# Performance work log

Measured on AMD Instinct MI355X. Metric: run time of the kernel, lower is better.

The kernel has to match this reference:

```python
import jax, jax.numpy as jnp
import numpy as np

N, HID, H, D = 2048, 1024, 16, 64


def setup_inputs() -> dict:
    key = jax.random.key(0)
    ks = jax.random.split(key, 10)
    s_in = 1.0 / np.sqrt(HID)      # Linear(hidden -> H*D) init scale
    s_o = 1.0 / np.sqrt(H * D)     # Linear(H*D -> D) init scale
    return {
        "x": jax.random.normal(ks[0], (N, HID), jnp.float32),
        "history": jnp.zeros((H, N, N), jnp.float32),
        "Wq_w": jax.random.uniform(ks[1], (H * D, HID), jnp.float32, -s_in, s_in),
        "Wq_b": jax.random.uniform(ks[2], (H * D,), jnp.float32, -s_in, s_in),
        "Wk_w": jax.random.uniform(ks[3], (H * D, HID), jnp.float32, -s_in, s_in),
        "Wk_b": jax.random.uniform(ks[4], (H * D,), jnp.float32, -s_in, s_in),
        "Wv_w": jax.random.uniform(ks[5], (H * D, HID), jnp.float32, -s_in, s_in),
        "Wv_b": jax.random.uniform(ks[6], (H * D,), jnp.float32, -s_in, s_in),
        "Wo_w": jax.random.uniform(ks[7], (D, H * D), jnp.float32, -s_o, s_o),
        "Wo_b": jax.random.uniform(ks[8], (D,), jnp.float32, -s_o, s_o),
        "beta": jnp.float32(0.1),
    }


def reference(x, history, Wq_w, Wq_b, Wk_w, Wk_b, Wv_w, Wv_b, Wo_w, Wo_b, beta):
    n = x.shape[0]
    # QKV projections: [N, H*D] -> [H, N, D]
    q = (x @ Wq_w.T + Wq_b).reshape(n, H, D).transpose(1, 0, 2)
    k = (x @ Wk_w.T + Wk_b).reshape(n, H, D).transpose(1, 0, 2)
    v = (x @ Wv_w.T + Wv_b).reshape(n, H, D).transpose(1, 0, 2)
    scores = jnp.einsum('hnd,hmd->hnm', q, k) / np.sqrt(D).astype(np.float32)
    scores = scores + beta * history  # learned additive history bias
    attn = jax.nn.softmax(scores, axis=-1)  # [H, N, N]
    new_history = history + jax.lax.stop_gradient(attn)  # stateful accumulation (detached)
    out = jnp.einsum('hnm,hmd->hnd', attn, v)  # [H, N, D]
    out = out.transpose(1, 0, 2).reshape(n, H * D)
    out = out @ Wo_w.T + Wo_b  # [N, D]
    # dropout is identity (p=0.0 / eval)
    return (out, attn, new_history)
```

## Files before the change

### kernel.cpp

```cpp
#include <hip/hip_runtime.h>
#include <hip/hip_bf16.h>

#define N_TOK 2048
#define HIDDEN 1024
#define NHEAD 16
#define DHEAD 64

typedef __attribute__((ext_vector_type(8))) short bf16x8;
typedef __attribute__((ext_vector_type(4))) float f32x4;

__device__ inline unsigned short f2bf(float x) {
    __hip_bfloat16 h = __float2bfloat16(x);
    return *reinterpret_cast<unsigned short*>(&h);
}

__device__ inline f32x4 zero4() {
    f32x4 z;
    z[0] = 0.f; z[1] = 0.f; z[2] = 0.f; z[3] = 0.f;
    return z;
}

__global__ void cvt4_kernel(const float* __restrict__ x, const float* __restrict__ wq,
                            const float* __restrict__ wk, const float* __restrict__ wv,
                            unsigned short* __restrict__ dst) {
    int i = blockIdx.x * blockDim.x + threadIdx.x;
    const float* src;
    int off;
    if (i < 524288)       { src = x;  off = i; }
    else if (i < 786432)  { src = wq; off = i - 524288; }
    else if (i < 1048576) { src = wk; off = i - 786432; }
    else                  { src = wv; off = i - 1048576; }
    float4 v = reinterpret_cast<const float4*>(src)[off];
    ushort4 o;
    o.x = f2bf(v.x); o.y = f2bf(v.y); o.z = f2bf(v.z); o.w = f2bf(v.w);
    reinterpret_cast<ushort4*>(dst)[i] = o;
}

__launch_bounds__(256)
__global__ void gemm_qkv(const unsigned short* __restrict__ xb,
                         const unsigned short* __restrict__ wb,
                         const float* __restrict__ bq, const float* __restrict__ bk,
                         const float* __restrict__ bv,
                         unsigned short* __restrict__ qb, unsigned short* __restrict__ kb,
                         unsigned short* __restrict__ vb) {
    __shared__ unsigned short As[2][128 * 64];
    __shared__ unsigned short Bs[2][128 * 64];
    const int tid = threadIdx.x;
    const int lane = tid & 63;
    const int w = tid >> 6;
    const int wr = w >> 1, wc = w & 1;
    const int rb = blockIdx.y * 128;
    const int cb = blockIdx.x * 128;
    const int r0 = tid >> 3, c0 = tid & 7;

    f32x4 acc[4][4];
    for (int i = 0; i < 4; i++)
        for (int j = 0; j < 4; j++) acc[i][j] = zero4();

    uint4 va[4], vb4[4];
#pragma unroll
    for (int i = 0; i < 4; i++) {
        va[i]  = *reinterpret_cast<const uint4*>(xb + (size_t)(rb + r0 + 32 * i) * HIDDEN + c0 * 8);
        vb4[i] = *reinterpret_cast<const uint4*>(wb + (size_t)(cb + r0 + 32 * i) * HIDDEN + c0 * 8);
    }
#pragma unroll
    for (int i = 0; i < 4; i++) {
        int row = r0 + 32 * i;
        *reinterpret_cast<uint4*>(As[0] + row * 64 + ((c0 ^ (row & 7)) << 3)) = va[i];
        *reinterpret_cast<uint4*>(Bs[0] + row * 64 + ((c0 ^ (row & 7)) << 3)) = vb4[i];
    }
    __syncthreads();
    int cur = 0;

    for (int kt = 0; kt < 16; ++kt) {
        if (kt < 15) {
#pragma unroll
            for (int i = 0; i < 4; i++) {
                va[i]  = *reinterpret_cast<const uint4*>(xb + (size_t)(rb + r0 + 32 * i) * HIDDEN + (kt + 1) * 64 + c0 * 8);
                vb4[i] = *reinterpret_cast<const uint4*>(wb + (size_t)(cb + r0 + 32 * i) * HIDDEN + (kt + 1) * 64 + c0 * 8);
            }
        }
#pragma unroll
        for (int kk = 0; kk < 2; kk++) {
            bf16x8 a[4], b[4];
#pragma unroll
            for (int mi = 0; mi < 4; mi++) {
                int row = wr * 64 + mi * 16 + (lane & 15);
                a[mi] = *reinterpret_cast<const bf16x8*>(As[cur] + row * 64 + (((kk * 4 + (lane >> 4)) ^ (row & 7)) << 3));
            }
#pragma unroll
            for (int ni = 0; ni < 4; ni++) {
                int row = wc * 64 + ni * 16 + (lane & 15);
                b[ni] = *reinterpret_cast<const bf16x8*>(Bs[cur] + row * 64 + (((kk * 4 + (lane >> 4)) ^ (row & 7)) << 3));
            }
#pragma unroll
            for (int mi = 0; mi < 4; mi++)
#pragma unroll
                for (int ni = 0; ni < 4; ni++)
                    acc[mi][ni] = __builtin_amdgcn_mfma_f32_16x16x32_bf16(a[mi], b[ni], acc[mi][ni], 0, 0, 0);
        }
        if (kt < 15) {
#pragma unroll
            for (int i = 0; i < 4; i++) {
                int row = r0 + 32 * i;
                *reinterpret_cast<uint4*>(As[cur ^ 1] + row * 64 + ((c0 ^ (row & 7)) << 3)) = va[i];
                *reinterpret_cast<uint4*>(Bs[cur ^ 1] + row * 64 + ((c0 ^ (row & 7)) << 3)) = vb4[i];
            }
        }
        __syncthreads();
        cur ^= 1;
    }

    const int region = blockIdx.x >> 3;
    const float* bias = region == 0 ? bq : (region == 1 ? bk : bv);
    unsigned short* dst = region == 0 ? qb : (region == 1 ? kb : vb);
#pragma unroll
    for (int mi = 0; mi < 4; mi++) {
#pragma unroll
        for (int ni = 0; ni < 4; ni++) {
            int colg = cb + wc * 64 + ni * 16 + (lane & 15);
            int jj = colg & 1023;
            int hh = jj >> 6, d = jj & 63;
            float bval = bias[jj];
#pragma unroll
            for (int r = 0; r < 4; r++) {
                int n = rb + wr * 64 + mi * 16 + ((lane >> 4) << 2) + r;
                dst[((size_t)hh * N_TOK + n) * 64 + d] = f2bf(acc[mi][ni][r] + bval);
            }
        }
    }
}

__global__ void transpose_v(const unsigned short* __restrict__ vb, unsigned short* __restrict__ vt) {
    int t = blockIdx.x * blockDim.x + threadIdx.x;
    int nc = t & 255, d = (t >> 8) & 63, h = t >> 14;
    int n0 = nc * 8;
    unsigned short tmp[8];
#pragma unroll
    for (int j = 0; j < 8; j++)
        tmp[j] = vb[((size_t)h * N_TOK + n0 + j) * 64 + d];
    size_t dsti = (((size_t)(h * 32 + (nc >> 3)) * 64 + d) * 64) + (nc & 7) * 8;
    *reinterpret_cast<uint4*>(vt + dsti) = *reinterpret_cast<uint4*>(tmp);
}

__launch_bounds__(64, 2)
__global__ void attn_fused(const unsigned short* __restrict__ qb,
                           const unsigned short* __restrict__ kb,
                           const unsigned short* __restrict__ vt,
                           const float* __restrict__ hist,
                           const float* __restrict__ beta_p,
                           float* __restrict__ attn_out,
                           float* __restrict__ nh_out,
                           float* __restrict__ hv) {
    __shared__ unsigned short Ks[64 * 64];
    __shared__ unsigned short Vs[64 * 64];
    __shared__ unsigned short Ps[16 * 64];
    const int lane = threadIdx.x;
    const int g = lane >> 4, q15 = lane & 15;
    const int jr8 = lane >> 3, jc = lane & 7;
    const int rb = blockIdx.x, h = blockIdx.y;
    const float beta = beta_p[0];
    const float scale = 0.125f;

    const unsigned short* qsrc = qb + ((size_t)h * N_TOK + rb * 16 + q15) * 64;
    bf16x8 aq0 = *reinterpret_cast<const bf16x8*>(qsrc + 8 * g);
    bf16x8 aq1 = *reinterpret_cast<const bf16x8*>(qsrc + 8 * g + 32);

    const unsigned short* kt0 = kb + (size_t)h * N_TOK * 64;
    const unsigned short* vt0 = vt + (size_t)h * 32 * 4096;
    const float* hbase = hist + ((size_t)h * N_TOK + rb * 16 + q15) * N_TOK + 4 * g;
    float* abase = attn_out + ((size_t)h * N_TOK + rb * 16 + q15) * N_TOK + 4 * g;
    float* nbase = nh_out + ((size_t)h * N_TOK + rb * 16 + q15) * N_TOK + 4 * g;

    float m = -1e30f, l = 0.0f;
    f32x4 h4[4], h4n[4];

    {
        uint4 kr[8];
#pragma unroll
        for (int i = 0; i < 8; i++)
            kr[i] = *reinterpret_cast<const uint4*>(kt0 + (size_t)(i * 8 + jr8) * 64 + jc * 8);
#pragma unroll
        for (int i = 0; i < 8; i++) {
            int row = i * 8 + jr8;
            *reinterpret_cast<uint4*>(Ks + row * 64 + ((jc ^ (row & 7)) << 3)) = kr[i];
        }
#pragma unroll
        for (int nt = 0; nt < 4; nt++) h4[nt] = *reinterpret_cast<const f32x4*>(hbase + nt * 16);
    }

    for (int t = 0; t < 32; t++) {
        uint4 kn[8];
        if (t < 31) {
#pragma unroll
            for (int i = 0; i < 8; i++)
                kn[i] = *reinterpret_cast<const uint4*>(kt0 + (size_t)(t + 1) * 4096 + (size_t)(i * 8 + jr8) * 64 + jc * 8);
#pragma unroll
            for (int nt = 0; nt < 4; nt++)
                h4n[nt] = *reinterpret_cast<const f32x4*>(hbase + (t + 1) * 64 + nt * 16);
        }
        f32x4 s_acc[4];
#pragma unroll
        for (int nt = 0; nt < 4; nt++) {
            int krow = nt * 16 + q15;
            bf16x8 kf0 = *reinterpret_cast<const bf16x8*>(Ks + krow * 64 + ((g ^ (q15 & 7)) << 3));
            bf16x8 kf1 = *reinterpret_cast<const bf16x8*>(Ks + krow * 64 + (((4 + g) ^ (q15 & 7)) << 3));
            s_acc[nt] = __builtin_amdgcn_mfma_f32_16x16x32_bf16(kf0, aq0, zero4(), 0, 0, 0);
            s_acc[nt] = __builtin_amdgcn_mfma_f32_16x16x32_bf16(kf1, aq1, s_acc[nt], 0, 0, 0);
        }
        float sc[4][4];
#pragma unroll
        for (int nt = 0; nt < 4; nt++)
#pragma unroll
            for (int r = 0; r < 4; r++)
                sc[nt][r] = s_acc[nt][r] * scale + beta * h4[nt][r];

        float tm = sc[0][0];
#pragma unroll
        for (int nt = 0; nt < 4; nt++)
#pragma unroll
            for (int r = 0; r < 4; r++) tm = fmaxf(tm, sc[nt][r]);
        tm = fmaxf(tm, __shfl_xor(tm, 16));
        tm = fmaxf(tm, __shfl_xor(tm, 32));
        float mn = fmaxf(m, tm);
        float ps = 0.0f;
#pragma unroll
        for (int nt = 0; nt < 4; nt++)
#pragma unroll
            for (int r = 0; r < 4; r++) ps += __expf(sc[nt][r] - mn);
        ps += __shfl_xor(ps, 16);
        ps += __shfl_xor(ps, 32);
        l = l * __expf(m - mn) + ps;
        m = mn;

        if (t < 31) {
#pragma unroll
            for (int i = 0; i < 8; i++) {
                int row = i * 8 + jr8;
                *reinterpret_cast<uint4*>(Ks + row * 64 + ((jc ^ (row & 7)) << 3)) = kn[i];
            }
#pragma unroll
            for (int nt = 0; nt < 4; nt++) h4[nt] = h4n[nt];
        }
    }
    const float inv_l = 1.0f / l;

    f32x4 oacc[4];
#pragma unroll
    for (int di = 0; di < 4; di++) oacc[di] = zero4();

    {
        uint4 vr[8];
#pragma unroll
        for (int i = 0; i < 8; i++)
            vr[i] = *reinterpret_cast<const uint4*>(vt0 + (size_t)31 * 4096 + (size_t)(i * 8 + jr8) * 64 + jc * 8);
#pragma unroll
        for (int i = 0; i < 8; i++) {
            int row = i * 8 + jr8;
            *reinterpret_cast<uint4*>(Vs + row * 64 + ((jc ^ (row & 7)) << 3)) = vr[i];
        }
#pragma unroll
        for (int nt = 0; nt < 4; nt++)
            h4[nt] = *reinterpret_cast<const f32x4*>(hbase + 31 * 64 + nt * 16);
    }

    for (int tt = 0; tt < 32; tt++) {
        const int t = 31 - tt;
        uint4 kn[8], vn[8];
        if (tt < 31) {
#pragma unroll
            for (int i = 0; i < 8; i++) {
                kn[i] = *reinterpret_cast<const uint4*>(kt0 + (size_t)(t - 1) * 4096 + (size_t)(i * 8 + jr8) * 64 + jc * 8);
                vn[i] = *reinterpret_cast<const uint4*>(vt0 + (size_t)(t - 1) * 4096 + (size_t)(i * 8 + jr8) * 64 + jc * 8);
            }
#pragma unroll
            for (int nt = 0; nt < 4; nt++)
                h4n[nt] = *reinterpret_cast<const f32x4*>(hbase + (t - 1) * 64 + nt * 16);
        }

        f32x4 s_acc[4];
#pragma unroll
        for (int nt = 0; nt < 4; nt++) {
            int krow = nt * 16 + q15;
            bf16x8 kf0 = *reinterpret_cast<const bf16x8*>(Ks + krow * 64 + ((g ^ (q15 & 7)) << 3));
            bf16x8 kf1 = *reinterpret_cast<const bf16x8*>(Ks + krow * 64 + (((4 + g) ^ (q15 & 7)) << 3));
            s_acc[nt] = __builtin_amdgcn_mfma_f32_16x16x32_bf16(kf0, aq0, zero4(), 0, 0, 0);
            s_acc[nt] = __builtin_amdgcn_mfma_f32_16x16x32_bf16(kf1, aq1, s_acc[nt], 0, 0, 0);
        }

#pragma unroll
        for (int nt = 0; nt < 4; nt++) {
            float a0 = __expf(s_acc[nt][0] * scale + beta * h4[nt][0] - m) * inv_l;
            float a1 = __expf(s_acc[nt][1] * scale + beta * h4[nt][1] - m) * inv_l;
            float a2 = __expf(s_acc[nt][2] * scale + beta * h4[nt][2] - m) * inv_l;
            float a3 = __expf(s_acc[nt][3] * scale + beta * h4[nt][3] - m) * inv_l;
            f32x4 av, nv;
            av[0] = a0; av[1] = a1; av[2] = a2; av[3] = a3;
            nv[0] = a0 + h4[nt][0]; nv[1] = a1 + h4[nt][1];
            nv[2] = a2 + h4[nt][2]; nv[3] = a3 + h4[nt][3];
            __builtin_nontemporal_store(av, reinterpret_cast<f32x4*>(abase + t * 64 + nt * 16));
            __builtin_nontemporal_store(nv, reinterpret_cast<f32x4*>(nbase + t * 64 + nt * 16));
            ushort4 p;
            p.x = f2bf(a0); p.y = f2bf(a1); p.z = f2bf(a2); p.w = f2bf(a3);
            *reinterpret_cast<ushort4*>(Ps + q15 * 64 + (((4 * nt + g) ^ (q15 & 14)) << 2)) = p;
        }

#pragma unroll
        for (int kk2 = 0; kk2 < 2; kk2++) {
            bf16x8 pa = *reinterpret_cast<const bf16x8*>(Ps + q15 * 64 + (((8 * kk2 + 2 * g) ^ (q15 & 14)) << 2));
#pragma unroll
            for (int di = 0; di < 4; di++) {
                int vrow = di * 16 + q15;
                bf16x8 vf = *reinterpret_cast<const bf16x8*>(Vs + vrow * 64 + (((kk2 * 4 + g) ^ (q15 & 7)) << 3));
                oacc[di] = __builtin_amdgcn_mfma_f32_16x16x32_bf16(pa, vf, oacc[di], 0, 0, 0);
            }
        }

        if (tt < 31) {
#pragma unroll
            for (int i = 0; i < 8; i++) {
                int row = i * 8 + jr8;
                *reinterpret_cast<uint4*>(Ks + row * 64 + ((jc ^ (row & 7)) << 3)) = kn[i];
                *reinterpret_cast<uint4*>(Vs + row * 64 + ((jc ^ (row & 7)) << 3)) = vn[i];
            }
#pragma unroll
            for (int nt = 0; nt < 4; nt++) h4[nt] = h4n[nt];
        }
    }

#pragma unroll
    for (int di = 0; di < 4; di++) {
#pragma unroll
        for (int r = 0; r < 4; r++) {
            int rl = g * 4 + r;
            int d = di * 16 + q15;
            hv[((size_t)h * N_TOK + rb * 16 + rl) * 64 + d] = oacc[di][r];
        }
    }
}

__launch_bounds__(256)
__global__ void out_proj(const float* __restrict__ hv, const float* __restrict__ Wo,
                         const float* __restrict__ bo, float* __restrict__ out) {
    __shared__ float wos[64][129];
    const int tid = threadIdx.x;
    const int dd = tid & 63;
    const int w = tid >> 6;
    const int n0 = blockIdx.x * 16;
    float acc[4] = {0.f, 0.f, 0.f, 0.f};
    for (int kc = 0; kc < 1024; kc += 128) {
        __syncthreads();
#pragma unroll
        for (int i = 0; i < 32; i++) {
            int e = tid + 256 * i;
            int r = e >> 7, j = e & 127;
            wos[r][j] = Wo[(size_t)r * 1024 + kc + j];
        }
        __syncthreads();
#pragma unroll 4
        for (int k = 0; k < 128; k++) {
            float wv = wos[dd][k];
            int jg = kc + k;
            const float* hb = hv + ((size_t)(jg >> 6) * N_TOK) * 64 + (jg & 63);
#pragma unroll
            for (int q = 0; q < 4; q++) {
                acc[q] += hb[(size_t)(n0 + w + 4 * q) * 64] * wv;
            }
        }
    }
#pragma unroll
    for (int q = 0; q < 4; q++)
        out[(size_t)(n0 + w + 4 * q) * 64 + dd] = acc[q] + bo[dd];
}

extern "C" void kernel_launch(void* const* d_in, const int* in_sizes, int n_in,
                              void* d_out, int out_size, void* d_ws, size_t ws_size,
                              hipStream_t stream) {
    const float* x    = (const float*)d_in[0];
    const float* hist = (const float*)d_in[1];
    const float* Wq_w = (const float*)d_in[2];
    const float* Wq_b = (const float*)d_in[3];
    const float* Wk_w = (const float*)d_in[4];
    const float* Wk_b = (const float*)d_in[5];
    const float* Wv_w = (const float*)d_in[6];
    const float* Wv_b = (const float*)d_in[7];
    const float* Wo_w = (const float*)d_in[8];
    const float* Wo_b = (const float*)d_in[9];
    const float* beta = (const float*)d_in[10];

    float* out = (float*)d_out;
    float* attn_out = out + 131072;
    float* nh_out = attn_out + (size_t)NHEAD * N_TOK * N_TOK;

    unsigned short* xb  = (unsigned short*)d_ws;
    unsigned short* wb  = xb + (size_t)N_TOK * HIDDEN;
    unsigned short* qb  = wb + (size_t)3 * HIDDEN * HIDDEN;
    unsigned short* kb  = qb + (size_t)N_TOK * HIDDEN;
    unsigned short* vb  = kb + (size_t)N_TOK * HIDDEN;
    unsigned short* vt  = vb + (size_t)N_TOK * HIDDEN;
    float* hvb = (float*)(vt + (size_t)N_TOK * HIDDEN);

    cvt4_kernel<<<5120, 256, 0, stream>>>(x, Wq_w, Wk_w, Wv_w, xb);
    gemm_qkv<<<dim3(24, 16), 256, 0, stream>>>(xb, wb, Wq_b, Wk_b, Wv_b, qb, kb, vb);
    transpose_v<<<1024, 256, 0, stream>>>(vb, vt);
    attn_fused<<<dim3(128, 16), 64, 0, stream>>>(qb, kb, vt, hist, beta,
                                                 attn_out, nh_out, hvb);
    out_proj<<<128, 256, 0, stream>>>(hvb, Wo_w, Wo_b, out);
}
```

Measured before the change: 550.3 us.

## Split attention key range across two waves per block with merged softmax stats

Each attention block now has two wavefronts, and each one handles half of every 64-key tile: 32 columns of K, V and history. The waves merge their running max and sum through shared memory before the second pass. At the end, the second wave's partial PV accumulator is added into the first wave's result through shared memory. The V transpose layout changes to 32-key sub-tiles to match. The goal is more in-flight waves and memory parallelism for the bandwidth-bound history read and attention writes, at the cost of two block syncs, extra shared memory traffic and half-width MFMA work per wave.

Result: no change. 557.7 us (+1.3%).

```diff
diff --git a/kernel.cpp b/kernel.cpp
--- a/kernel.cpp
+++ b/kernel.cpp
@@ -139,11 +139,11 @@
 #pragma unroll
     for (int j = 0; j < 8; j++)
         tmp[j] = vb[((size_t)h * N_TOK + n0 + j) * 64 + d];
-    size_t dsti = (((size_t)(h * 32 + (nc >> 3)) * 64 + d) * 64) + (nc & 7) * 8;
+    size_t dsti = (((size_t)(h * 64 + (nc >> 2)) * 64 + d) * 32) + (nc & 3) * 8;
     *reinterpret_cast<uint4*>(vt + dsti) = *reinterpret_cast<uint4*>(tmp);
 }
 
-__launch_bounds__(64, 2)
+__launch_bounds__(128, 4)
 __global__ void attn_fused(const unsigned short* __restrict__ qb,
                            const unsigned short* __restrict__ kb,
                            const unsigned short* __restrict__ vt,
@@ -152,72 +152,77 @@
                            float* __restrict__ attn_out,
                            float* __restrict__ nh_out,
                            float* __restrict__ hv) {
-    __shared__ unsigned short Ks[64 * 64];
-    __shared__ unsigned short Vs[64 * 64];
-    __shared__ unsigned short Ps[16 * 64];
-    const int lane = threadIdx.x;
+    __shared__ unsigned short SH[2][4608];
+    const int tid = threadIdx.x;
+    const int w = tid >> 6;
+    const int lane = tid & 63;
     const int g = lane >> 4, q15 = lane & 15;
-    const int jr8 = lane >> 3, jc = lane & 7;
+    const int jr = lane >> 3, jc = lane & 7;
+    const int jrv = lane >> 2, jcv = lane & 3;
     const int rb = blockIdx.x, h = blockIdx.y;
     const float beta = beta_p[0];
     const float scale = 0.125f;
 
+    unsigned short* Ksw = SH[w];
+    unsigned short* Vsw = SH[w] + 2048;
+    unsigned short* Psw = SH[w] + 4096;
+
     const unsigned short* qsrc = qb + ((size_t)h * N_TOK + rb * 16 + q15) * 64;
     bf16x8 aq0 = *reinterpret_cast<const bf16x8*>(qsrc + 8 * g);
     bf16x8 aq1 = *reinterpret_cast<const bf16x8*>(qsrc + 8 * g + 32);
 
-    const unsigned short* kt0 = kb + (size_t)h * N_TOK * 64;
-    const unsigned short* vt0 = vt + (size_t)h * 32 * 4096;
-    const float* hbase = hist + ((size_t)h * N_TOK + rb * 16 + q15) * N_TOK + 4 * g;
-    float* abase = attn_out + ((size_t)h * N_TOK + rb * 16 + q15) * N_TOK + 4 * g;
-    float* nbase = nh_out + ((size_t)h * N_TOK + rb * 16 + q15) * N_TOK + 4 * g;
+    const unsigned short* kt0 = kb + (size_t)h * N_TOK * 64 + w * 2048;
+    const unsigned short* vt0 = vt + ((size_t)(h * 64 + w)) * 2048;
+    const float* hbase = hist + ((size_t)h * N_TOK + rb * 16 + q15) * N_TOK + w * 32 + 4 * g;
+    float* abase = attn_out + ((size_t)h * N_TOK + rb * 16 + q15) * N_TOK + w * 32 + 4 * g;
+    float* nbase = nh_out + ((size_t)h * N_TOK + rb * 16 + q15) * N_TOK + w * 32 + 4 * g;
 
     float m = -1e30f, l = 0.0f;
-    f32x4 h4[4], h4n[4];
+    f32x4 h4[2], h4n[2];
 
     {
-        uint4 kr[8];
-#pragma unroll
-        for (int i = 0; i < 8; i++)
-            kr[i] = *reinterpret_cast<const uint4*>(kt0 + (size_t)(i * 8 + jr8) * 64 + jc * 8);
-#pragma unroll
-        for (int i = 0; i < 8; i++) {
-            int row = i * 8 + jr8;
-            *reinterpret_cast<uint4*>(Ks + row * 64 + ((jc ^ (row & 7)) << 3)) = kr[i];
-        }
-#pragma unroll
-        for (int nt = 0; nt < 4; nt++) h4[nt] = *reinterpret_cast<const f32x4*>(hbase + nt * 16);
+        uint4 kr[4];
+#pragma unroll
+        for (int i = 0; i < 4; i++)
+            kr[i] = *reinterpret_cast<const uint4*>(kt0 + (size_t)(i * 8 + jr) * 64 + jc * 8);
+#pragma unroll
+        for (int i = 0; i < 4; i++) {
+            int row = i * 8 + jr;
+            *reinterpret_cast<uint4*>(Ksw + row * 64 + ((jc ^ (row & 7)) << 3)) = kr[i];
+        }
+#pragma unroll
+        for (int nt = 0; nt < 2; nt++) h4[nt] = *reinterpret_cast<const f32x4*>(hbase + nt * 16);
     }
 
     for (int t = 0; t < 32; t++) {
-        uint4 kn[8];
+        uint4 kn[4];
         if (t < 31) {
 #pragma unroll
-            for (int i = 0; i < 8; i++)
-                kn[i] = *reinterpret_cast<const uint4*>(kt0 + (size_t)(t + 1) * 4096 + (size_t)(i * 8 + jr8) * 64 + jc * 8);
-#pragma unroll
-            for (int nt = 0; nt < 4; nt++)
+            for (int i = 0; i < 4; i++)
+                kn[i] = *reinterpret_cast<const uint4*>(kt0 + (size_t)(t + 1) * 4096 + (size_t)(i * 8 + jr) * 64 + jc * 8);
+#pragma unroll
+            for (int nt = 0; nt < 2; nt++)
                 h4n[nt] = *reinterpret_cast<const f32x4*>(hbase + (t + 1) * 64 + nt * 16);
         }
-        f32x4 s_acc[4];
-#pragma unroll
-        for (int nt = 0; nt < 4; nt++) {
+        f32x4 s_acc[2];
+#pragma unroll
+        for (int nt = 0; nt < 2; nt++) {
             int krow = nt * 16 + q15;
-            bf16x8 kf0 = *reinterpret_cast<const bf16x8*>(Ks + krow * 64 + ((g ^ (q15 & 7)) << 3));
-            bf16x8 kf1 = *reinterpret_cast<const bf16x8*>(Ks + krow * 64 + (((4 + g) ^ (q15 & 7)) << 3));
+            bf16x8 kf0 = *reinterpret_cast<const bf16x8*>(Ksw + krow * 64 + ((g ^ (q15 & 7)) << 3));
+            bf16x8 kf1 = *reinterpret_cast<const bf16x8*>(Ksw + krow * 64 + (((4 + g) ^ (q15 & 7)) << 3));
             s_acc[nt] = __builtin_amdgcn_mfma_f32_16x16x32_bf16(kf0, aq0, zero4(), 0, 0, 0);
             s_acc[nt] = __builtin_amdgcn_mfma_f32_16x16x32_bf16(kf1, aq1, s_acc[nt], 0, 0, 0);
         }
-        float sc[4][4];
-#pragma unroll
-        for (int nt = 0; nt < 4; nt++)
+        float sc[2][4];
+#pragma unroll
+        for (int nt = 0; nt < 2; nt++)
 #pragma unroll
             for (int r = 0; r < 4; r++)
                 sc[nt][r] = s_acc[nt][r] * scale + beta * h4[nt][r];
 
         float tm = sc[0][0];
 #pragma unroll
-        for (int nt = 0; nt < 4; nt++)
+        for (int nt = 0; nt < 2; nt++)
 #pragma unroll
             for (int r = 0; r < 4; r++) tm = fmaxf(tm, sc[nt][r]);
         tm = fmaxf(tm, __shfl_xor(tm, 16));
@@ -225,7 +230,7 @@
         float mn = fmaxf(m, tm);
         float ps = 0.0f;
 #pragma unroll
-        for (int nt = 0; nt < 4; nt++)
+        for (int nt = 0; nt < 2; nt++)
 #pragma unroll
             for (int r = 0; r < 4; r++) ps += __expf(sc[nt][r] - mn);
         ps += __shfl_xor(ps, 16);
@@ -235,61 +240,77 @@
 
         if (t < 31) {
 #pragma unroll
-            for (int i = 0; i < 8; i++) {
-                int row = i * 8 + jr8;
-                *reinterpret_cast<uint4*>(Ks + row * 64 + ((jc ^ (row & 7)) << 3)) = kn[i];
-            }
-#pragma unroll
-            for (int nt = 0; nt < 4; nt++) h4[nt] = h4n[nt];
-        }
-    }
-    const float inv_l = 1.0f / l;
+            for (int i = 0; i < 4; i++) {
+                int row = i * 8 + jr;
+                *reinterpret_cast<uint4*>(Ksw + row * 64 + ((jc ^ (row & 7)) << 3)) = kn[i];
+            }
+#pragma unroll
+            for (int nt = 0; nt < 2; nt++) h4[nt] = h4n[nt];
+        }
+    }
+
+    float inv_l;
+    {
+        float* mlbuf = (float*)(SH[0] + 4096);
+        if (g == 0) {
+            mlbuf[w * 16 + q15] = m;
+            mlbuf[32 + w * 16 + q15] = l;
+        }
+        __syncthreads();
+        float m0 = mlbuf[q15], m1 = mlbuf[16 + q15];
+        float l0 = mlbuf[32 + q15], l1 = mlbuf[48 + q15];
+        float gm = fmaxf(m0, m1);
+        float gl = l0 * __expf(m0 - gm) + l1 * __expf(m1 - gm);
+        m = gm;
+        inv_l = 1.0f / gl;
+        __syncthreads();
+    }
 
     f32x4 oacc[4];
 #pragma unroll
     for (int di = 0; di < 4; di++) oacc[di] = zero4();
 
     {
-        uint4 vr[8];
-#pragma unroll
-        for (int i = 0; i < 8; i++)
-            vr[i] = *reinterpret_cast<const uint4*>(vt0 + (size_t)31 * 4096 + (size_t)(i * 8 + jr8) * 64 + jc * 8);
-#pragma unroll
-        for (int i = 0; i < 8; i++) {
-            int row = i * 8 + jr8;
-            *reinterpret_cast<uint4*>(Vs + row * 64 + ((jc ^ (row & 7)) << 3)) = vr[i];
-        }
-#pragma unroll
-        for (int nt = 0; nt < 4; nt++)
+        uint4 vr[4];
+#pragma unroll
+        for (int i = 0; i < 4; i++)
+            vr[i] = *reinterpret_cast<const uint4*>(vt0 + (size_t)31 * 4096 + (size_t)(i * 16 + jrv) * 32 + jcv * 8);
+#pragma unroll
+        for (int i = 0; i < 4; i++) {
+            int row = i * 16 + jrv;
+            *reinterpret_cast<uint4*>(Vsw + row * 32 + ((jcv ^ ((row >> 1) & 3)) << 3)) = vr[i];
+        }
+#pragma unroll
+        for (int nt = 0; nt < 2; nt++)
             h4[nt] = *reinterpret_cast<const f32x4*>(hbase + 31 * 64 + nt * 16);
     }
 
     for (int tt = 0; tt < 32; tt++) {
         const int t = 31 - tt;
-        uint4 kn[8], vn[8];
+        uint4 kn[4], vn[4];
         if (tt < 31) {
 #pragma unroll
-            for (int i = 0; i < 8; i++) {
-                kn[i] = *reinterpret_cast<const uint4*>(kt0 + (size_t)(t - 1) * 4096 + (size_t)(i * 8 + jr8) * 64 + jc * 8);
-                vn[i] = *reinterpret_cast<const uint4*>(vt0 + (size_t)(t - 1) * 4096 + (size_t)(i * 8 + jr8) * 64 + jc * 8);
-            }
-#pragma unroll
-            for (int nt = 0; nt < 4; nt++)
+            for (int i = 0; i < 4; i++) {
+                kn[i] = *reinterpret_cast<const uint4*>(kt0 + (size_t)(t - 1) * 4096 + (size_t)(i * 8 + jr) * 64 + jc * 8);
+                vn[i] = *reinterpret_cast<const uint4*>(vt0 + (size_t)(t - 1) * 4096 + (size_t)(i * 16 + jrv) * 32 + jcv * 8);
+            }
+#pragma unroll
+            for (int nt = 0; nt < 2; nt++)
                 h4n[nt] = *reinterpret_cast<const f32x4*>(hbase + (t - 1) * 64 + nt * 16);
         }
 
-        f32x4 s_acc[4];
-#pragma unroll
-        for (int nt = 0; nt < 4; nt++) {
+        f32x4 s_acc[2];
+#pragma unroll
+        for (int nt = 0; nt < 2; nt++) {
             int krow = nt * 16 + q15;
-            bf16x8 kf0 = *reinterpret_cast<const bf16x8*>(Ks + krow * 64 + ((g ^ (q15 & 7)) << 3));
-            bf16x8 kf1 = *reinterpret_cast<const bf16x8*>(Ks + krow * 64 + (((4 + g) ^ (q15 & 7)) << 3));
+            bf16x8 kf0 = *reinterpret_cast<const bf16x8*>(Ksw + krow * 64 + ((g ^ (q15 & 7)) << 3));
+            bf16x8 kf1 = *reinterpret_cast<const bf16x8*>(Ksw + krow * 64 + (((4 + g) ^ (q15 & 7)) << 3));
             s_acc[nt] = __builtin_amdgcn_mfma_f32_16x16x32_bf16(kf0, aq0, zero4(), 0, 0, 0);
             s_acc[nt] = __builtin_amdgcn_mfma_f32_16x16x32_bf16(kf1, aq1, s_acc[nt], 0, 0, 0);
         }
 
 #pragma unroll
-        for (int nt = 0; nt < 4; nt++) {
+        for (int nt = 0; nt < 2; nt++) {
             float a0 = __expf(s_acc[nt][0] * scale + beta * h4[nt][0] - m) * inv_l;
             float a1 = __expf(s_acc[nt][1] * scale + beta * h4[nt][1] - m) * inv_l;
             float a2 = __expf(s_acc[nt][2] * scale + beta * h4[nt][2] - m) * inv_l;
@@ -302,39 +323,56 @@
             __builtin_nontemporal_store(nv, reinterpret_cast<f32x4*>(nbase + t * 64 + nt * 16));
             ushort4 p;
             p.x = f2bf(a0); p.y = f2bf(a1); p.z = f2bf(a2); p.w = f2bf(a3);
-            *reinterpret_cast<ushort4*>(Ps + q15 * 64 + (((4 * nt + g) ^ (q15 & 14)) << 2)) = p;
-        }
-
-#pragma unroll
-        for (int kk2 = 0; kk2 < 2; kk2++) {
-            bf16x8 pa = *reinterpret_cast<const bf16x8*>(Ps + q15 * 64 + (((8 * kk2 + 2 * g) ^ (q15 & 14)) << 2));
+            *reinterpret_cast<ushort4*>(Psw + q15 * 32 + (((4 * nt + g) ^ (q15 & 6)) << 2)) = p;
+        }
+
+        {
+            bf16x8 pa = *reinterpret_cast<const bf16x8*>(Psw + q15 * 32 + (((2 * g) ^ (q15 & 6)) << 2));
 #pragma unroll
             for (int di = 0; di < 4; di++) {
                 int vrow = di * 16 + q15;
-                bf16x8 vf = *reinterpret_cast<const bf16x8*>(Vs + vrow * 64 + (((kk2 * 4 + g) ^ (q15 & 7)) << 3));
+                bf16x8 vf = *reinterpret_cast<const bf16x8*>(Vsw + vrow * 32 + ((g ^ ((q15 >> 1) & 3)) << 3));
                 oacc[di] = __builtin_amdgcn_mfma_f32_16x16x32_bf16(pa, vf, oacc[di], 0, 0, 0);
             }
         }
 
         if (tt < 31) {
 #pragma unroll
-            for (int i = 0; i < 8; i++) {
-                int row = i * 8 + jr8;
-                *reinterpret_cast<uint4*>(Ks + row * 64 + ((jc ^ (row & 7)) << 3)) = kn[i];
-                *reinterpret_cast<uint4*>(Vs + row * 64 + ((jc ^ (row & 7)) << 3)) = vn[i];
-            }
-#pragma unroll
-            for (int nt = 0; nt < 4; nt++) h4[nt] = h4n[nt];
-        }
-    }
-
-#pragma unroll
-    for (int di = 0; di < 4; di++) {
-#pragma unroll
-        for (int r = 0; r < 4; r++) {
-            int rl = g * 4 + r;
-            int d = di * 16 + q15;
-            hv[((size_t)h * N_TOK + rb * 16 + rl) * 64 + d] = oacc[di][r];
+            for (int i = 0; i < 4; i++) {
+                int row = i * 8 + jr;
+                *reinterpret_cast<uint4*>(Ksw + row * 64 + ((jc ^ (row & 7)) << 3)) = kn[i];
+            }
+#pragma unroll
+            for (int i = 0; i < 4; i++) {
+                int row = i * 16 + jrv;
+                *reinterpret_cast<uint4*>(Vsw + row * 32 + ((jcv ^ ((row >> 1) & 3)) << 3)) = vn[i];
+            }
+#pragma unroll
+            for (int nt = 0; nt < 2; nt++) h4[nt] = h4n[nt];
+        }
+    }
+
+    {
+        float* vbuf = (float*)(SH[1] + 2048);
+        if (w == 1) {
+#pragma unroll
+            for (int di = 0; di < 4; di++)
+#pragma unroll
+                for (int r = 0; r < 4; r++)
+                    vbuf[(4 * g + r) * 64 + di * 16 + q15] = oacc[di][r];
+        }
+        __syncthreads();
+        if (w == 0) {
+#pragma unroll
+            for (int di = 0; di < 4; di++) {
+#pragma unroll
+                for (int r = 0; r < 4; r++) {
+                    int rl = 4 * g + r;
+                    int d = di * 16 + q15;
+                    hv[((size_t)h * N_TOK + rb * 16 + rl) * 64 + d] =
+                        oacc[di][r] + vbuf[rl * 64 + d];
+                }
+            }
         }
     }
 }
@@ -403,7 +441,7 @@
     cvt4_kernel<<<5120, 256, 0, stream>>>(x, Wq_w, Wk_w, Wv_w, xb);
     gemm_qkv<<<dim3(24, 16), 256, 0, stream>>>(xb, wb, Wq_b, Wk_b, Wv_b, qb, kb, vb);
     transpose_v<<<1024, 256, 0, stream>>>(vb, vt);
-    attn_fused<<<dim3(128, 16), 64, 0, stream>>>(qb, kb, vt, hist, beta,
-                                                 attn_out, nh_out, hvb);
+    attn_fused<<<dim3(128, 16), 128, 0, stream>>>(qb, kb, vt, hist, beta,
+                                                  attn_out, nh_out, hvb);
     out_proj<<<128, 256, 0, stream>>>(hvb, Wo_w, Wo_b, out);
 }
```

## Stream K/V via direct global-to-LDS loads with double buffering and fuse V transpose

Applied to the files above, without the earlier changes.

The attention kernel now uses global_load_lds to copy K and V tiles straight into double-buffered LDS. Tiles shrink to 32 keys, and explicit vmcnt waits replace the register staging and rewrite steps. The V transpose moves into the QKV GEMM epilogue, which removes a separate kernel and its intermediate buffer. The attention grid is flattened and block IDs are remapped so blocks are interleaved across heads, and the output stores are deferred by one iteration to overlap them with loads. The risks are hand-counted waitcnt values, which are fragile if the compiler reorders memory operations, and scattered 2-byte writes for the transposed V in the GEMM epilogue.

Result: faster. 520.7 us (-5.4%).

```diff
diff --git a/kernel.cpp b/kernel.cpp
--- a/kernel.cpp
+++ b/kernel.cpp
@@ -9,6 +9,9 @@
 typedef __attribute__((ext_vector_type(8))) short bf16x8;
 typedef __attribute__((ext_vector_type(4))) float f32x4;
 
+#define WAITV(N) do { asm volatile("s_waitcnt vmcnt(" #N ")" ::: "memory"); \
+                      __builtin_amdgcn_sched_barrier(0); } while (0)
+
 __device__ inline unsigned short f2bf(float x) {
     __hip_bfloat16 h = __float2bfloat16(x);
     return *reinterpret_cast<unsigned short*>(&h);
@@ -18,6 +21,12 @@
     f32x4 z;
     z[0] = 0.f; z[1] = 0.f; z[2] = 0.f; z[3] = 0.f;
     return z;
+}
+
+__device__ inline void gl_lds16(const unsigned short* g, unsigned short* l) {
+    __builtin_amdgcn_global_load_lds(
+        (const __attribute__((address_space(1))) unsigned int*)g,
+        (__attribute__((address_space(3))) unsigned int*)l, 16, 0, 0);
 }
 
 __global__ void cvt4_kernel(const float* __restrict__ x, const float* __restrict__ wq,
@@ -42,7 +51,7 @@
                          const float* __restrict__ bq, const float* __restrict__ bk,
                          const float* __restrict__ bv,
                          unsigned short* __restrict__ qb, unsigned short* __restrict__ kb,
-                         unsigned short* __restrict__ vb) {
+                         unsigned short* __restrict__ vt) {
     __shared__ unsigned short As[2][128 * 64];
     __shared__ unsigned short Bs[2][128 * 64];
     const int tid = threadIdx.x;
@@ -113,7 +122,7 @@
 
     const int region = blockIdx.x >> 3;
     const float* bias = region == 0 ? bq : (region == 1 ? bk : bv);
-    unsigned short* dst = region == 0 ? qb : (region == 1 ? kb : vb);
+    unsigned short* dst = region == 0 ? qb : kb;
 #pragma unroll
     for (int mi = 0; mi < 4; mi++) {
 #pragma unroll
@@ -125,22 +134,14 @@
 #pragma unroll
             for (int r = 0; r < 4; r++) {
                 int n = rb + wr * 64 + mi * 16 + ((lane >> 4) << 2) + r;
-                dst[((size_t)hh * N_TOK + n) * 64 + d] = f2bf(acc[mi][ni][r] + bval);
-            }
-        }
-    }
-}
-
-__global__ void transpose_v(const unsigned short* __restrict__ vb, unsigned short* __restrict__ vt) {
-    int t = blockIdx.x * blockDim.x + threadIdx.x;
-    int nc = t & 255, d = (t >> 8) & 63, h = t >> 14;
-    int n0 = nc * 8;
-    unsigned short tmp[8];
-#pragma unroll
-    for (int j = 0; j < 8; j++)
-        tmp[j] = vb[((size_t)h * N_TOK + n0 + j) * 64 + d];
-    size_t dsti = (((size_t)(h * 32 + (nc >> 3)) * 64 + d) * 64) + (nc & 7) * 8;
-    *reinterpret_cast<uint4*>(vt + dsti) = *reinterpret_cast<uint4*>(tmp);
+                unsigned short val = f2bf(acc[mi][ni][r] + bval);
+                if (region < 2)
+                    dst[((size_t)hh * N_TOK + n) * 64 + d] = val;
+                else
+                    vt[(((size_t)(hh * 64 + (n >> 5)) * 64 + d) * 32) + (n & 31)] = val;
+            }
+        }
+    }
 }
 
 __launch_bounds__(64, 2)
@@ -152,13 +153,14 @@
                            float* __restrict__ attn_out,
                            float* __restrict__ nh_out,
                            float* __restrict__ hv) {
-    __shared__ unsigned short Ks[64 * 64];
-    __shared__ unsigned short Vs[64 * 64];
-    __shared__ unsigned short Ps[16 * 64];
+    __shared__ unsigned short Kbuf[2][2048];
+    __shared__ unsigned short Vbuf[2][2048];
+    __shared__ unsigned short Psw[512];
     const int lane = threadIdx.x;
     const int g = lane >> 4, q15 = lane & 15;
-    const int jr8 = lane >> 3, jc = lane & 7;
-    const int rb = blockIdx.x, h = blockIdx.y;
+    const int bid = blockIdx.x;
+    const int orig = (bid & 7) * 256 + (bid >> 3);
+    const int h = orig >> 7, rb = orig & 127;
     const float beta = beta_p[0];
     const float scale = 0.125f;
 
@@ -166,130 +168,119 @@
     bf16x8 aq0 = *reinterpret_cast<const bf16x8*>(qsrc + 8 * g);
     bf16x8 aq1 = *reinterpret_cast<const bf16x8*>(qsrc + 8 * g + 32);
 
+    const int koff = (lane >> 3) * 64 + (((lane & 7) ^ (lane >> 3)) << 3);
+    const int voff = (lane >> 2) * 32 + (((lane & 3) ^ ((lane >> 3) & 3)) << 3);
     const unsigned short* kt0 = kb + (size_t)h * N_TOK * 64;
-    const unsigned short* vt0 = vt + (size_t)h * 32 * 4096;
-    const float* hbase = hist + ((size_t)h * N_TOK + rb * 16 + q15) * N_TOK + 4 * g;
-    float* abase = attn_out + ((size_t)h * N_TOK + rb * 16 + q15) * N_TOK + 4 * g;
-    float* nbase = nh_out + ((size_t)h * N_TOK + rb * 16 + q15) * N_TOK + 4 * g;
+    const unsigned short* vt0 = vt + (size_t)h * N_TOK * 64;
+
+#define STAGE_K(T, B) do { const unsigned short* _s = kt0 + (size_t)(T) * 2048 + koff; \
+        gl_lds16(_s,        &Kbuf[B][0]);    gl_lds16(_s + 512,  &Kbuf[B][512]);   \
+        gl_lds16(_s + 1024, &Kbuf[B][1024]); gl_lds16(_s + 1536, &Kbuf[B][1536]); } while (0)
+#define STAGE_V(T, B) do { const unsigned short* _s = vt0 + (size_t)(T) * 2048 + voff; \
+        gl_lds16(_s,        &Vbuf[B][0]);    gl_lds16(_s + 512,  &Vbuf[B][512]);   \
+        gl_lds16(_s + 1024, &Vbuf[B][1024]); gl_lds16(_s + 1536, &Vbuf[B][1536]); } while (0)
+
+    const size_t rowbase = ((size_t)h * N_TOK + rb * 16 + q15) * N_TOK;
+    const float* hbase = hist + rowbase + 4 * g;
+    float* abase = attn_out + rowbase + 4 * g;
+    float* nbase = nh_out + rowbase + 4 * g;
 
     float m = -1e30f, l = 0.0f;
-    f32x4 h4[4], h4n[4];
-
-    {
-        uint4 kr[8];
-#pragma unroll
-        for (int i = 0; i < 8; i++)
-            kr[i] = *reinterpret_cast<const uint4*>(kt0 + (size_t)(i * 8 + jr8) * 64 + jc * 8);
-#pragma unroll
-        for (int i = 0; i < 8; i++) {
-            int row = i * 8 + jr8;
-            *reinterpret_cast<uint4*>(Ks + row * 64 + ((jc ^ (row & 7)) << 3)) = kr[i];
-        }
-#pragma unroll
-        for (int nt = 0; nt < 4; nt++) h4[nt] = *reinterpret_cast<const f32x4*>(hbase + nt * 16);
-    }
-
-    for (int t = 0; t < 32; t++) {
-        uint4 kn[8];
-        if (t < 31) {
-#pragma unroll
-            for (int i = 0; i < 8; i++)
-                kn[i] = *reinterpret_cast<const uint4*>(kt0 + (size_t)(t + 1) * 4096 + (size_t)(i * 8 + jr8) * 64 + jc * 8);
-#pragma unroll
-            for (int nt = 0; nt < 4; nt++)
-                h4n[nt] = *reinterpret_cast<const f32x4*>(hbase + (t + 1) * 64 + nt * 16);
-        }
-        f32x4 s_acc[4];
-#pragma unroll
-        for (int nt = 0; nt < 4; nt++) {
+    f32x4 h4[2], h4n[2];
+
+    STAGE_K(0, 0);
+    h4[0] = *reinterpret_cast<const f32x4*>(hbase);
+    h4[1] = *reinterpret_cast<const f32x4*>(hbase + 16);
+
+    for (int t = 0; t < 64; ++t) {
+        const int cur = t & 1;
+        if (t < 63) {
+            STAGE_K(t + 1, cur ^ 1);
+            h4n[0] = *reinterpret_cast<const f32x4*>(hbase + (t + 1) * 32);
+            h4n[1] = *reinterpret_cast<const f32x4*>(hbase + (t + 1) * 32 + 16);
+            WAITV(6);
+        } else {
+            WAITV(0);
+        }
+        f32x4 s_acc[2];
+#pragma unroll
+        for (int nt = 0; nt < 2; ++nt) {
             int krow = nt * 16 + q15;
-            bf16x8 kf0 = *reinterpret_cast<const bf16x8*>(Ks + krow * 64 + ((g ^ (q15 & 7)) << 3));
-            bf16x8 kf1 = *reinterpret_cast<const bf16x8*>(Ks + krow * 64 + (((4 + g) ^ (q15 & 7)) << 3));
+            bf16x8 kf0 = *reinterpret_cast<const bf16x8*>(Kbuf[cur] + krow * 64 + ((g ^ (q15 & 7)) << 3));
+            bf16x8 kf1 = *reinterpret_cast<const bf16x8*>(Kbuf[cur] + krow * 64 + (((4 + g) ^ (q15 & 7)) << 3));
             s_acc[nt] = __builtin_amdgcn_mfma_f32_16x16x32_bf16(kf0, aq0, zero4(), 0, 0, 0);
             s_acc[nt] = __builtin_amdgcn_mfma_f32_16x16x32_bf16(kf1, aq1, s_acc[nt], 0, 0, 0);
         }
-        float sc[4][4];
-#pragma unroll
-        for (int nt = 0; nt < 4; nt++)
-#pragma unroll
-            for (int r = 0; r < 4; r++)
+        float sc[2][4];
+#pragma unroll
+        for (int nt = 0; nt < 2; ++nt)
+#pragma unroll
+            for (int r = 0; r < 4; ++r)
                 sc[nt][r] = s_acc[nt][r] * scale + beta * h4[nt][r];
 
         float tm = sc[0][0];
 #pragma unroll
-        for (int nt = 0; nt < 4; nt++)
-#pragma unroll
-            for (int r = 0; r < 4; r++) tm = fmaxf(tm, sc[nt][r]);
+        for (int nt = 0; nt < 2; ++nt)
+#pragma unroll
+            for (int r = 0; r < 4; ++r) tm = fmaxf(tm, sc[nt][r]);
         tm = fmaxf(tm, __shfl_xor(tm, 16));
         tm = fmaxf(tm, __shfl_xor(tm, 32));
         float mn = fmaxf(m, tm);
         float ps = 0.0f;
 #pragma unroll
-        for (int nt = 0; nt < 4; nt++)
-#pragma unroll
-            for (int r = 0; r < 4; r++) ps += __expf(sc[nt][r] - mn);
+        for (int nt = 0; nt < 2; ++nt)
+#pragma unroll
+            for (int r = 0; r < 4; ++r) ps += __expf(sc[nt][r] - mn);
         ps += __shfl_xor(ps, 16);
         ps += __shfl_xor(ps, 32);
         l = l * __expf(m - mn) + ps;
         m = mn;
 
-        if (t < 31) {
-#pragma unroll
-            for (int i = 0; i < 8; i++) {
-                int row = i * 8 + jr8;
-                *reinterpret_cast<uint4*>(Ks + row * 64 + ((jc ^ (row & 7)) << 3)) = kn[i];
-            }
-#pragma unroll
-            for (int nt = 0; nt < 4; nt++) h4[nt] = h4n[nt];
-        }
+        h4[0] = h4n[0]; h4[1] = h4n[1];
     }
     const float inv_l = 1.0f / l;
 
     f32x4 oacc[4];
 #pragma unroll
-    for (int di = 0; di < 4; di++) oacc[di] = zero4();
-
-    {
-        uint4 vr[8];
-#pragma unroll
-        for (int i = 0; i < 8; i++)
-            vr[i] = *reinterpret_cast<const uint4*>(vt0 + (size_t)31 * 4096 + (size_t)(i * 8 + jr8) * 64 + jc * 8);
-#pragma unroll
-        for (int i = 0; i < 8; i++) {
-            int row = i * 8 + jr8;
-            *reinterpret_cast<uint4*>(Vs + row * 64 + ((jc ^ (row & 7)) << 3)) = vr[i];
-        }
-#pragma unroll
-        for (int nt = 0; nt < 4; nt++)
-            h4[nt] = *reinterpret_cast<const f32x4*>(hbase + 31 * 64 + nt * 16);
-    }
-
-    for (int tt = 0; tt < 32; tt++) {
-        const int t = 31 - tt;
-        uint4 kn[8], vn[8];
-        if (tt < 31) {
-#pragma unroll
-            for (int i = 0; i < 8; i++) {
-                kn[i] = *reinterpret_cast<const uint4*>(kt0 + (size_t)(t - 1) * 4096 + (size_t)(i * 8 + jr8) * 64 + jc * 8);
-                vn[i] = *reinterpret_cast<const uint4*>(vt0 + (size_t)(t - 1) * 4096 + (size_t)(i * 8 + jr8) * 64 + jc * 8);
-            }
-#pragma unroll
-            for (int nt = 0; nt < 4; nt++)
-                h4n[nt] = *reinterpret_cast<const f32x4*>(hbase + (t - 1) * 64 + nt * 16);
-        }
-
-        f32x4 s_acc[4];
-#pragma unroll
-        for (int nt = 0; nt < 4; nt++) {
+    for (int di = 0; di < 4; ++di) oacc[di] = zero4();
+
+    STAGE_V(63, 1);
+    h4[0] = *reinterpret_cast<const f32x4*>(hbase + 63 * 32);
+    h4[1] = *reinterpret_cast<const f32x4*>(hbase + 63 * 32 + 16);
+
+    f32x4 sa0, sa1, sn0, sn1;
+
+    for (int tt = 0; tt < 64; ++tt) {
+        const int t = 63 - tt;
+        const int cur = t & 1;
+        if (tt > 0) {
+            __builtin_nontemporal_store(sa0, reinterpret_cast<f32x4*>(abase + (t + 1) * 32));
+            __builtin_nontemporal_store(sa1, reinterpret_cast<f32x4*>(abase + (t + 1) * 32 + 16));
+            __builtin_nontemporal_store(sn0, reinterpret_cast<f32x4*>(nbase + (t + 1) * 32));
+            __builtin_nontemporal_store(sn1, reinterpret_cast<f32x4*>(nbase + (t + 1) * 32 + 16));
+        }
+        if (tt < 63) {
+            STAGE_K(t - 1, cur ^ 1);
+            STAGE_V(t - 1, cur ^ 1);
+            h4n[0] = *reinterpret_cast<const f32x4*>(hbase + (t - 1) * 32);
+            h4n[1] = *reinterpret_cast<const f32x4*>(hbase + (t - 1) * 32 + 16);
+        }
+        if (tt == 0)      { WAITV(10); }
+        else if (tt < 63) { WAITV(14); }
+        else              { WAITV(4);  }
+
+        f32x4 s_acc[2];
+#pragma unroll
+        for (int nt = 0; nt < 2; ++nt) {
             int krow = nt * 16 + q15;
-            bf16x8 kf0 = *reinterpret_cast<const bf16x8*>(Ks + krow * 64 + ((g ^ (q15 & 7)) << 3));
-            bf16x8 kf1 = *reinterpret_cast<const bf16x8*>(Ks + krow * 64 + (((4 + g) ^ (q15 & 7)) << 3));
+            bf16x8 kf0 = *reinterpret_cast<const bf16x8*>(Kbuf[cur] + krow * 64 + ((g ^ (q15 & 7)) << 3));
+            bf16x8 kf1 = *reinterpret_cast<const bf16x8*>(Kbuf[cur] + krow * 64 + (((4 + g) ^ (q15 & 7)) << 3));
             s_acc[nt] = __builtin_amdgcn_mfma_f32_16x16x32_bf16(kf0, aq0, zero4(), 0, 0, 0);
             s_acc[nt] = __builtin_amdgcn_mfma_f32_16x16x32_bf16(kf1, aq1, s_acc[nt], 0, 0, 0);
         }
 
 #pragma unroll
-        for (int nt = 0; nt < 4; nt++) {
+        for (int nt = 0; nt < 2; ++nt) {
             float a0 = __expf(s_acc[nt][0] * scale + beta * h4[nt][0] - m) * inv_l;
             float a1 = __expf(s_acc[nt][1] * scale + beta * h4[nt][1] - m) * inv_l;
             float a2 = __expf(s_acc[nt][2] * scale + beta * h4[nt][2] - m) * inv_l;
@@ -298,45 +289,40 @@
             av[0] = a0; av[1] = a1; av[2] = a2; av[3] = a3;
             nv[0] = a0 + h4[nt][0]; nv[1] = a1 + h4[nt][1];
             nv[2] = a2 + h4[nt][2]; nv[3] = a3 + h4[nt][3];
-            __builtin_nontemporal_store(av, reinterpret_cast<f32x4*>(abase + t * 64 + nt * 16));
-            __builtin_nontemporal_store(nv, reinterpret_cast<f32x4*>(nbase + t * 64 + nt * 16));
+            if (nt == 0) { sa0 = av; sn0 = nv; } else { sa1 = av; sn1 = nv; }
             ushort4 p;
             p.x = f2bf(a0); p.y = f2bf(a1); p.z = f2bf(a2); p.w = f2bf(a3);
-            *reinterpret_cast<ushort4*>(Ps + q15 * 64 + (((4 * nt + g) ^ (q15 & 14)) << 2)) = p;
-        }
-
-#pragma unroll
-        for (int kk2 = 0; kk2 < 2; kk2++) {
-            bf16x8 pa = *reinterpret_cast<const bf16x8*>(Ps + q15 * 64 + (((8 * kk2 + 2 * g) ^ (q15 & 14)) << 2));
-#pragma unroll
-            for (int di = 0; di < 4; di++) {
+            *reinterpret_cast<ushort4*>(Psw + q15 * 32 + (((4 * nt + g) ^ (q15 & 6)) << 2)) = p;
+        }
+
+        {
+            bf16x8 pa = *reinterpret_cast<const bf16x8*>(Psw + q15 * 32 + (((2 * g) ^ (q15 & 6)) << 2));
+#pragma unroll
+            for (int di = 0; di < 4; ++di) {
                 int vrow = di * 16 + q15;
-                bf16x8 vf = *reinterpret_cast<const bf16x8*>(Vs + vrow * 64 + (((kk2 * 4 + g) ^ (q15 & 7)) << 3));
+                bf16x8 vf = *reinterpret_cast<const bf16x8*>(Vbuf[cur] + vrow * 32 + ((g ^ ((q15 >> 1) & 3)) << 3));
                 oacc[di] = __builtin_amdgcn_mfma_f32_16x16x32_bf16(pa, vf, oacc[di], 0, 0, 0);
             }
         }
 
-        if (tt < 31) {
-#pragma unroll
-            for (int i = 0; i < 8; i++) {
-                int row = i * 8 + jr8;
-                *reinterpret_cast<uint4*>(Ks + row * 64 + ((jc ^ (row & 7)) << 3)) = kn[i];
-                *reinterpret_cast<uint4*>(Vs + row * 64 + ((jc ^ (row & 7)) << 3)) = vn[i];
-            }
-#pragma unroll
-            for (int nt = 0; nt < 4; nt++) h4[nt] = h4n[nt];
-        }
-    }
-
-#pragma unroll
-    for (int di = 0; di < 4; di++) {
-#pragma unroll
-        for (int r = 0; r < 4; r++) {
+        h4[0] = h4n[0]; h4[1] = h4n[1];
+    }
+    __builtin_nontemporal_store(sa0, reinterpret_cast<f32x4*>(abase));
+    __builtin_nontemporal_store(sa1, reinterpret_cast<f32x4*>(abase + 16));
+    __builtin_nontemporal_store(sn0, reinterpret_cast<f32x4*>(nbase));
+    __builtin_nontemporal_store(sn1, reinterpret_cast<f32x4*>(nbase + 16));
+
+#pragma unroll
+    for (int di = 0; di < 4; ++di) {
+#pragma unroll
+        for (int r = 0; r < 4; ++r) {
             int rl = g * 4 + r;
             int d = di * 16 + q15;
             hv[((size_t)h * N_TOK + rb * 16 + rl) * 64 + d] = oacc[di][r];
         }
     }
+#undef STAGE_K
+#undef STAGE_V
 }
 
 __launch_bounds__(256)
@@ -396,14 +382,11 @@
     unsigned short* wb  = xb + (size_t)N_TOK * HIDDEN;
     unsigned short* qb  = wb + (size_t)3 * HIDDEN * HIDDEN;
     unsigned short* kb  = qb + (size_t)N_TOK * HIDDEN;
-    unsigned short* vb  = kb + (size_t)N_TOK * HIDDEN;
-    unsigned short* vt  = vb + (size_t)N_TOK * HIDDEN;
+    unsigned short* vt  = kb + (size_t)N_TOK * HIDDEN;
     float* hvb = (float*)(vt + (size_t)N_TOK * HIDDEN);
 
     cvt4_kernel<<<5120, 256, 0, stream>>>(x, Wq_w, Wk_w, Wv_w, xb);
-    gemm_qkv<<<dim3(24, 16), 256, 0, stream>>>(xb, wb, Wq_b, Wk_b, Wv_b, qb, kb, vb);
-    transpose_v<<<1024, 256, 0, stream>>>(vb, vt);
-    attn_fused<<<dim3(128, 16), 64, 0, stream>>>(qb, kb, vt, hist, beta,
-                                                 attn_out, nh_out, hvb);
+    gemm_qkv<<<dim3(24, 16), 256, 0, stream>>>(xb, wb, Wq_b, Wk_b, Wv_b, qb, kb, vt);
+    attn_fused<<<2048, 64, 0, stream>>>(qb, kb, vt, hist, beta, attn_out, nh_out, hvb);
     out_proj<<<128, 256, 0, stream>>>(hvb, Wo_w, Wo_b, out);
 }
```
